# Kernel tuning notes

Measured on AMD Instinct MI355X. Metric: run time of the kernel, lower is better.

## Reference

```python
import jax, jax.numpy as jnp
import numpy as np

NUM_HEADS = 4

def setup_inputs() -> dict:
    key = jax.random.key(0)
    ks = jax.random.split(key, 5)
    B, T, F, C = 2, 128, 256, 256
    # weights scaled ~1/sqrt(C) so softmax is not saturated
    s = 1.0 / np.sqrt(C)
    return {
        "x": jax.random.normal(ks[0], (B, T, F, C), jnp.float32),
        "w_in": jax.random.normal(ks[1], (3 * C, C), jnp.float32) * s,
        "b_in": jax.random.normal(ks[2], (3 * C,), jnp.float32) * 0.01,
        "w_out": jax.random.normal(ks[3], (C, C), jnp.float32) * s,
        "b_out": jax.random.normal(ks[4], (C,), jnp.float32) * 0.01,
        "band": 16,
    }

def reference(x, w_in, b_in, w_out, b_out, band):
    B, T, F, C = x.shape
    H = NUM_HEADS
    D = C // H
    x2 = x.reshape(B * T, F, C)  # attention over frequency, independent per (B,T)
    qkv = x2 @ w_in.T + b_in  # [BT, F, 3C]
    q, k, v = jnp.split(qkv, 3, axis=-1)
    def heads(t):
        return t.reshape(B * T, F, H, D).transpose(0, 2, 1, 3)  # [BT, H, F, D]
    q, k, v = heads(q), heads(k), heads(v)
    scores = jnp.einsum('bhid,bhjd->bhij', q, k) / jnp.sqrt(jnp.asarray(D, x.dtype))
    i = jnp.arange(F)[:, None]
    j = jnp.arange(F)[None, :]
    keep = jnp.abs(i - j) <= band  # banded locality mask [F, F]
    scores = jnp.where(keep, scores, -jnp.inf)
    attn = jax.nn.softmax(scores, axis=-1)
    out = jnp.einsum('bhij,bhjd->bhid', attn, v)  # [BT, H, F, D]
    out = out.transpose(0, 2, 1, 3).reshape(B * T, F, C)
    y = out @ w_out.T + b_out
    return y.reshape(B, T, F, C)
```

## Files before the change

kernel.cpp:

```cpp
#include <hip/hip_runtime.h>
#include <hip/hip_bf16.h>
#include <cstdint>

typedef unsigned int u32;
typedef __attribute__((ext_vector_type(8))) __bf16 bf16x8;
typedef __attribute__((ext_vector_type(4))) float f32x4;
typedef __attribute__((ext_vector_type(2))) _Float16 half2_t;

#define BT_N 256
#define F_N 256
#define C_N 256
#define H_N 4
#define D_N 64
#define TC_N 768
#define M_N (BT_N * F_N)

__device__ __forceinline__ ushort f2bf(float f) {
  u32 u = __float_as_uint(f);
  u32 r = (u + 0x7fffu + ((u >> 16) & 1u)) >> 16;
  return (ushort)r;
}

__device__ __forceinline__ half2_t u2h(u32 u) {
  return __builtin_bit_cast(half2_t, u);
}

__device__ __forceinline__ void store_out(_Float16* p, float v) { *p = (_Float16)v; }
__device__ __forceinline__ void store_out(float* p, float v) { *p = v; }

__device__ __forceinline__ void gload_lds16(const ushort* g, ushort* l) {
  __builtin_amdgcn_global_load_lds(
      (const __attribute__((address_space(1))) u32*)g,
      (__attribute__((address_space(3))) u32*)l, 16, 0, 0);
}

__device__ __forceinline__ float dpp_xor1_add(float x) {
  int t = __builtin_amdgcn_mov_dpp(__builtin_bit_cast(int, x), 0xB1, 0xF, 0xF, true);
  return x + __builtin_bit_cast(float, t);
}
__device__ __forceinline__ float dpp_xor2_add(float x) {
  int t = __builtin_amdgcn_mov_dpp(__builtin_bit_cast(int, x), 0x4E, 0xF, 0xF, true);
  return x + __builtin_bit_cast(float, t);
}

__global__ __launch_bounds__(256) void cvt3_f32_bf16_k(
    const float* __restrict__ sx, ushort* __restrict__ dx, int nx4,
    const float* __restrict__ si, ushort* __restrict__ di, int ni4,
    const float* __restrict__ so, ushort* __restrict__ dq, int no4) {
  int idx = blockIdx.x * 256 + threadIdx.x;
  int stride = gridDim.x * 256;
  int ntot = nx4 + ni4 + no4;
  for (int i = idx; i < ntot; i += stride) {
    const float4* s;
    ushort* d;
    if (i < nx4) { s = (const float4*)sx + i; d = dx + (size_t)i * 4; }
    else if (i < nx4 + ni4) { int k = i - nx4; s = (const float4*)si + k; d = di + (size_t)k * 4; }
    else { int k = i - nx4 - ni4; s = (const float4*)so + k; d = dq + (size_t)k * 4; }
    float4 v = *s;
    u32 a = (u32)f2bf(v.x) | ((u32)f2bf(v.y) << 16);
    u32 b = (u32)f2bf(v.z) | ((u32)f2bf(v.w) << 16);
    *(uint2*)d = make_uint2(a, b);
  }
}

template <typename OutT>
__global__ __launch_bounds__(256, 2) void gemm_bt(
    const ushort* __restrict__ Ap, const ushort* __restrict__ Bp,
    const float* __restrict__ bias, OutT* __restrict__ Cp,
    int N, int NTN, int nwg8) {
  constexpr bool F32OUT = (sizeof(OutT) == 4);
  constexpr int SMEM_BYTES = F32OUT ? 67584 : 65536;
  __shared__ char smem[SMEM_BYTES];
  ushort* smemH = (ushort*)smem;

  const int tid = threadIdx.x;
  const int lane = tid & 63;
  const int wid = tid >> 6;
  const int wr = wid >> 1, wc = wid & 1;
  const int l15 = lane & 15, l4 = lane >> 4;
  const int b = blockIdx.x;
  const int bid = (b & 7) * nwg8 + (b >> 3);
  const int tm = bid / NTN;
  const int tn = bid - tm * NTN;
  const int rowBase = tm * 128, colBase = tn * 128;

  f32x4 acc[4][4] = {};

  const int ar = (tid >> 3);
  const int akk = (((tid & 7) ^ (ar & 7)) << 3);
  const ushort* gA = Ap + (size_t)(rowBase + ar) * 256 + akk;
  const ushort* gB = Bp + (size_t)(colBase + ar) * 256 + akk;

#define STAGE(buf, k0)                                                        \
  {                                                                           \
    ushort* As_ = smemH + (buf) * 8192;                                       \
    ushort* Bs_ = smemH + 16384 + (buf) * 8192;                               \
    _Pragma("unroll") for (int c = 0; c < 4; ++c) {                           \
      gload_lds16(gA + (size_t)(c * 32) * 256 + (k0),                         \
                  As_ + (size_t)(c * 256 + (wid << 6)) * 8);                  \
      gload_lds16(gB + (size_t)(c * 32) * 256 + (k0),                         \
                  Bs_ + (size_t)(c * 256 + (wid << 6)) * 8);                  \
    }                                                                         \
  }

  STAGE(0, 0);
  int cur = 0;
#pragma unroll
  for (int t = 0; t < 4; ++t) {
    __syncthreads();
    if (t < 3) STAGE(cur ^ 1, (t + 1) * 64);
    const ushort* As_ = smemH + cur * 8192;
    const ushort* Bs_ = smemH + 16384 + cur * 8192;
#pragma unroll
    for (int kk = 0; kk < 2; ++kk) {
      bf16x8 af[4];
      bf16x8 bfr[4];
#pragma unroll
      for (int i2 = 0; i2 < 4; ++i2) {
        int row = wr * 64 + i2 * 16 + l15;
        af[i2] = *(const bf16x8*)(As_ + row * 64 + (((kk * 4 + l4) ^ (l15 & 7)) * 8));
      }
#pragma unroll
      for (int j2 = 0; j2 < 4; ++j2) {
        int row = wc * 64 + j2 * 16 + l15;
        bfr[j2] = *(const bf16x8*)(Bs_ + row * 64 + (((kk * 4 + l4) ^ (l15 & 7)) * 8));
      }
#pragma unroll
      for (int i2 = 0; i2 < 4; ++i2)
#pragma unroll
        for (int j2 = 0; j2 < 4; ++j2)
          acc[i2][j2] = __builtin_amdgcn_mfma_f32_16x16x32_bf16(
              af[i2], bfr[j2], acc[i2][j2], 0, 0, 0);
    }
    cur ^= 1;
  }
#undef STAGE

  __syncthreads();
  if constexpr (F32OUT) {
    float* eb = (float*)smem;
#pragma unroll
    for (int j2 = 0; j2 < 4; ++j2) {
      float bv = bias[colBase + wc * 64 + j2 * 16 + l15];
#pragma unroll
      for (int i2 = 0; i2 < 4; ++i2)
#pragma unroll
        for (int r = 0; r < 4; ++r)
          eb[(wr * 64 + i2 * 16 + l4 * 4 + r) * 132 + wc * 64 + j2 * 16 + l15] =
              acc[i2][j2][r] + bv;
    }
    __syncthreads();
#pragma unroll
    for (int i = 0; i < 32; ++i) {
      int row = wid * 32 + i;
      uint2 d = *(const uint2*)((const u32*)eb + row * 132 + lane * 2);
      *(uint2*)((float*)Cp + (size_t)(rowBase + row) * N + colBase + lane * 2) = d;
    }
  } else {
    ushort* eb = smemH;
#pragma unroll
    for (int j2 = 0; j2 < 4; ++j2) {
      float bv = bias[colBase + wc * 64 + j2 * 16 + l15];
#pragma unroll
      for (int i2 = 0; i2 < 4; ++i2)
#pragma unroll
        for (int r = 0; r < 4; ++r) {
          _Float16 h = (_Float16)(acc[i2][j2][r] + bv);
          eb[(wr * 64 + i2 * 16 + l4 * 4 + r) * 136 + wc * 64 + j2 * 16 + l15] =
              __builtin_bit_cast(ushort, h);
        }
    }
    __syncthreads();
#pragma unroll
    for (int i = 0; i < 16; ++i) {
      int row = wid * 32 + 2 * i + (lane >> 5);
      int hl = lane & 31;
      uint2 d = *(const uint2*)(eb + row * 136 + hl * 4);
      *(uint2*)((_Float16*)Cp + (size_t)(rowBase + row) * N + colBase + hl * 4) = d;
    }
  }
}

__global__ __launch_bounds__(256) void attn_banded(
    const _Float16* __restrict__ qkv, ushort* __restrict__ aout) {
  __shared__ uint4 kbuf4[256 * 8];
  __shared__ uint4 vbuf4[256 * 8];
  const int tid = threadIdx.x;
  const int bt = blockIdx.x >> 2;
  const int h = blockIdx.x & 3;
  const _Float16* base = qkv + (size_t)bt * F_N * TC_N + h * D_N;

  {
    const int r0 = tid >> 3;
    const int c = tid & 7;
    const int cs = c ^ ((tid >> 5) & 7);
#pragma unroll
    for (int p = 0; p < 8; ++p) {
      int r = p * 32 + r0;
      uint4 k4 = *(const uint4*)(base + (size_t)r * TC_N + 256 + c * 8);
      uint4 v4 = *(const uint4*)(base + (size_t)r * TC_N + 512 + c * 8);
      kbuf4[r * 8 + cs] = k4;
      vbuf4[r * 8 + cs] = v4;
    }
  }

  const int q = tid >> 2;
  const int s = tid & 3;

  half2_t qh[4][8];
#pragma unroll
  for (int ii = 0; ii < 4; ++ii) {
    const uint4* gq = (const uint4*)(base + (size_t)(4 * q + ii) * TC_N + s * 16);
    uint4 a = gq[0], b2 = gq[1];
    qh[ii][0] = u2h(a.x); qh[ii][1] = u2h(a.y); qh[ii][2] = u2h(a.z); qh[ii][3] = u2h(a.w);
    qh[ii][4] = u2h(b2.x); qh[ii][5] = u2h(b2.y); qh[ii][6] = u2h(b2.z); qh[ii][7] = u2h(b2.w);
  }
  __syncthreads();

  float l[4] = {0.f, 0.f, 0.f, 0.f};
  half2_t o[4][8];
  const _Float16 z0 = (_Float16)0.f;
#pragma unroll
  for (int ii = 0; ii < 4; ++ii)
#pragma unroll
    for (int m = 0; m < 8; ++m) o[ii][m] = half2_t{z0, z0};

#pragma unroll 4
  for (int jo = 0; jo < 36; ++jo) {
    int j = 4 * q - 16 + jo;
    int jc = j < 0 ? 0 : (j > 255 ? 255 : j);
    int cb = (jc >> 2) & 7;
    const uint4* krow = kbuf4 + jc * 8;
    uint4 ka = krow[(2 * s) ^ cb];
    uint4 kb = krow[(2 * s + 1) ^ cb];
    half2_t kh[8];
    kh[0] = u2h(ka.x); kh[1] = u2h(ka.y); kh[2] = u2h(ka.z); kh[3] = u2h(ka.w);
    kh[4] = u2h(kb.x); kh[5] = u2h(kb.y); kh[6] = u2h(kb.z); kh[7] = u2h(kb.w);

    float dv[4];
#pragma unroll
    for (int ii = 0; ii < 4; ++ii) {
      float a0 = 0.f, a1 = 0.f;
#pragma unroll
      for (int m = 0; m < 4; ++m) {
        a0 = __builtin_amdgcn_fdot2(kh[2 * m], qh[ii][2 * m], a0, false);
        a1 = __builtin_amdgcn_fdot2(kh[2 * m + 1], qh[ii][2 * m + 1], a1, false);
      }
      dv[ii] = a0 + a1;
    }
#pragma unroll
    for (int ii = 0; ii < 4; ++ii) {
      dv[ii] = dpp_xor1_add(dv[ii]);
      dv[ii] = dpp_xor2_add(dv[ii]);
    }

    bool okj = (j >= 0) && (j < 256);
    float p[4];
    p[0] = (okj && jo <= 32) ? __expf(dv[0] * 0.125f) : 0.f;
    p[1] = (okj && jo >= 1 && jo <= 33) ? __expf(dv[1] * 0.125f) : 0.f;
    p[2] = (okj && jo >= 2 && jo <= 34) ? __expf(dv[2] * 0.125f) : 0.f;
    p[3] = (okj && jo >= 3) ? __expf(dv[3] * 0.125f) : 0.f;

    const uint4* vrow = vbuf4 + jc * 8;
    uint4 va = vrow[(2 * s) ^ cb];
    uint4 vb = vrow[(2 * s + 1) ^ cb];
    half2_t vh[8];
    vh[0] = u2h(va.x); vh[1] = u2h(va.y); vh[2] = u2h(va.z); vh[3] = u2h(va.w);
    vh[4] = u2h(vb.x); vh[5] = u2h(vb.y); vh[6] = u2h(vb.z); vh[7] = u2h(vb.w);

#pragma unroll
    for (int ii = 0; ii < 4; ++ii) {
      l[ii] += p[ii];
      _Float16 pf = (_Float16)p[ii];
      half2_t ph = {pf, pf};
#pragma unroll
      for (int m = 0; m < 8; ++m) o[ii][m] = vh[m] * ph + o[ii][m];
    }
  }

#pragma unroll
  for (int ii = 0; ii < 4; ++ii) {
    float inv = 1.f / l[ii];
    u32 w[4];
#pragma unroll
    for (int m = 0; m < 4; ++m) {
      float f0 = (float)o[ii][2 * m][0] * inv;
      float f1 = (float)o[ii][2 * m][1] * inv;
      float f2 = (float)o[ii][2 * m + 1][0] * inv;
      float f3 = (float)o[ii][2 * m + 1][1] * inv;
      w[m] = 0;
      w[m] = (u32)f2bf(f0) | ((u32)f2bf(f1) << 16);
      ((u32*)w)[m] = w[m];
      u32 hi = (u32)f2bf(f2) | ((u32)f2bf(f3) << 16);
      if (m & 1) { }
      w[m] = w[m];
      u32* dst = (u32*)(aout + (size_t)(bt * F_N + 4 * q + ii) * C_N + h * D_N + s * 16) + 2 * m;
      dst[0] = w[m];
      dst[1] = hi;
    }
  }
}

extern "C" void kernel_launch(void* const* d_in, const int* in_sizes, int n_in,
                              void* d_out, int out_size, void* d_ws, size_t ws_size,
                              hipStream_t stream) {
  const float* x = (const float*)d_in[0];
  const float* w_in = (const float*)d_in[1];
  const float* b_in = (const float*)d_in[2];
  const float* w_out = (const float*)d_in[3];
  const float* b_out = (const float*)d_in[4];
  float* y = (float*)d_out;

  char* ws = (char*)d_ws;
  const size_t qkv_bytes = (size_t)M_N * TC_N * 2;
  const size_t xb_bytes = (size_t)M_N * C_N * 2;
  _Float16* qkv = (_Float16*)ws;
  ushort* xb = (ushort*)(ws + qkv_bytes);
  ushort* attn = xb;
  ushort* winb = (ushort*)(ws + qkv_bytes + xb_bytes);
  ushort* woutb = winb + TC_N * C_N;

  cvt3_f32_bf16_k<<<2048, 256, 0, stream>>>(x, xb, M_N * C_N / 4,
                                            w_in, winb, TC_N * C_N / 4,
                                            w_out, woutb, C_N * C_N / 4);

  gemm_bt<_Float16><<<(M_N / 128) * (TC_N / 128), 256, 0, stream>>>(
      xb, winb, b_in, qkv, TC_N, TC_N / 128, (M_N / 128) * (TC_N / 128) / 8);

  attn_banded<<<BT_N * H_N, 256, 0, stream>>>(qkv, attn);

  gemm_bt<float><<<(M_N / 128) * (C_N / 128), 256, 0, stream>>>(
      attn, woutb, b_out, y, C_N, C_N / 128, (M_N / 128) * (C_N / 128) / 8);
}
```

Measured before the change: 120.5 us.

## Rewrite banded attention kernel with MFMA 16x16x16 f16 tiles

Replaces the scalar fdot2 banded attention with a matrix-core version. Each wave handles 64 query rows as four 16-row tiles, computes QK^T over three 16-key tiles covering the band with MFMA, and applies a precomputed bitmask, exp2 with folded scale, and a shuffle-reduced row sum. V is stored transposed in LDS so P·V can also use MFMA. This computes some wasted products outside the band and adds transposed scalar LDS stores, but it moves the main arithmetic onto matrix cores.

```diff
diff --git a/kernel.cpp b/kernel.cpp
--- a/kernel.cpp
+++ b/kernel.cpp
@@ -6,6 +6,8 @@
 typedef __attribute__((ext_vector_type(8))) __bf16 bf16x8;
 typedef __attribute__((ext_vector_type(4))) float f32x4;
 typedef __attribute__((ext_vector_type(2))) _Float16 half2_t;
+typedef __attribute__((ext_vector_type(4))) _Float16 half4;
+typedef __attribute__((ext_vector_type(2))) __fp16 fp16x2;
 
 #define BT_N 256
 #define F_N 256
@@ -14,6 +16,7 @@
 #define D_N 64
 #define TC_N 768
 #define M_N (BT_N * F_N)
+#define VT_ST 268
 
 __device__ __forceinline__ ushort f2bf(float f) {
   u32 u = __float_as_uint(f);
@@ -21,26 +24,10 @@
   return (ushort)r;
 }
 
-__device__ __forceinline__ half2_t u2h(u32 u) {
-  return __builtin_bit_cast(half2_t, u);
-}
-
-__device__ __forceinline__ void store_out(_Float16* p, float v) { *p = (_Float16)v; }
-__device__ __forceinline__ void store_out(float* p, float v) { *p = v; }
-
 __device__ __forceinline__ void gload_lds16(const ushort* g, ushort* l) {
   __builtin_amdgcn_global_load_lds(
       (const __attribute__((address_space(1))) u32*)g,
       (__attribute__((address_space(3))) u32*)l, 16, 0, 0);
-}
-
-__device__ __forceinline__ float dpp_xor1_add(float x) {
-  int t = __builtin_amdgcn_mov_dpp(__builtin_bit_cast(int, x), 0xB1, 0xF, 0xF, true);
-  return x + __builtin_bit_cast(float, t);
-}
-__device__ __forceinline__ float dpp_xor2_add(float x) {
-  int t = __builtin_amdgcn_mov_dpp(__builtin_bit_cast(int, x), 0x4E, 0xF, 0xF, true);
-  return x + __builtin_bit_cast(float, t);
 }
 
 __global__ __launch_bounds__(256) void cvt3_f32_bf16_k(
@@ -181,122 +168,126 @@
   }
 }
 
-__global__ __launch_bounds__(256) void attn_banded(
+__global__ __launch_bounds__(256) void attn_mfma(
     const _Float16* __restrict__ qkv, ushort* __restrict__ aout) {
-  __shared__ uint4 kbuf4[256 * 8];
-  __shared__ uint4 vbuf4[256 * 8];
+  __shared__ ushort smem[18432 + 64 * VT_ST];
   const int tid = threadIdx.x;
   const int bt = blockIdx.x >> 2;
   const int h = blockIdx.x & 3;
-  const _Float16* base = qkv + (size_t)bt * F_N * TC_N + h * D_N;
+  const _Float16* base = qkv + (size_t)bt * 256 * 768 + h * 64;
+  ushort* klds = smem;
+  ushort* vlds = smem + 18432;
 
   {
-    const int r0 = tid >> 3;
-    const int c = tid & 7;
-    const int cs = c ^ ((tid >> 5) & 7);
+    const int r0 = tid >> 3, c8 = tid & 7;
 #pragma unroll
     for (int p = 0; p < 8; ++p) {
-      int r = p * 32 + r0;
-      uint4 k4 = *(const uint4*)(base + (size_t)r * TC_N + 256 + c * 8);
-      uint4 v4 = *(const uint4*)(base + (size_t)r * TC_N + 512 + c * 8);
-      kbuf4[r * 8 + cs] = k4;
-      vbuf4[r * 8 + cs] = v4;
-    }
-  }
-
-  const int q = tid >> 2;
-  const int s = tid & 3;
-
-  half2_t qh[4][8];
-#pragma unroll
-  for (int ii = 0; ii < 4; ++ii) {
-    const uint4* gq = (const uint4*)(base + (size_t)(4 * q + ii) * TC_N + s * 16);
-    uint4 a = gq[0], b2 = gq[1];
-    qh[ii][0] = u2h(a.x); qh[ii][1] = u2h(a.y); qh[ii][2] = u2h(a.z); qh[ii][3] = u2h(a.w);
-    qh[ii][4] = u2h(b2.x); qh[ii][5] = u2h(b2.y); qh[ii][6] = u2h(b2.z); qh[ii][7] = u2h(b2.w);
-  }
+      int j = p * 32 + r0;
+      const uint4 k4 = *(const uint4*)(base + (size_t)j * 768 + 256 + c8 * 8);
+      *(uint4*)(klds + j * 72 + c8 * 8) = k4;
+      const uint4 v4 = *(const uint4*)(base + (size_t)j * 768 + 512 + c8 * 8);
+      const ushort* vh = (const ushort*)&v4;
+      ushort* vtp = vlds + (c8 * 8) * VT_ST + j;
+#pragma unroll
+      for (int i = 0; i < 8; ++i) vtp[i * VT_ST] = vh[i];
+    }
+  }
+
+  const int w = tid >> 6, lane = tid & 63;
+  const int l15 = lane & 15, g = lane >> 4, g4 = g * 4;
+
+  uint2 qf0[4], qf1[4], qf2[4], qf3[4];
+  {
+    const uint2* q0 = (const uint2*)(base + (size_t)(w * 64 + 0 * 16 + l15) * 768 + g4);
+    const uint2* q1 = (const uint2*)(base + (size_t)(w * 64 + 1 * 16 + l15) * 768 + g4);
+    const uint2* q2 = (const uint2*)(base + (size_t)(w * 64 + 2 * 16 + l15) * 768 + g4);
+    const uint2* q3 = (const uint2*)(base + (size_t)(w * 64 + 3 * 16 + l15) * 768 + g4);
+#pragma unroll
+    for (int ks = 0; ks < 4; ++ks) {
+      qf0[ks] = q0[ks * 4]; qf1[ks] = q1[ks * 4];
+      qf2[ks] = q2[ks * 4]; qf3[ks] = q3[ks * 4];
+    }
+  }
+
+  u32 bb = 0;
+#pragma unroll
+  for (int jt = 0; jt < 3; ++jt)
+#pragma unroll
+    for (int r = 0; r < 4; ++r) {
+      int d = 16 * jt + g4 + r - 16 - l15;
+      if (d >= -16 && d <= 16) bb |= 1u << (jt * 4 + r);
+    }
+
   __syncthreads();
 
-  float l[4] = {0.f, 0.f, 0.f, 0.f};
-  half2_t o[4][8];
-  const _Float16 z0 = (_Float16)0.f;
-#pragma unroll
-  for (int ii = 0; ii < 4; ++ii)
-#pragma unroll
-    for (int m = 0; m < 8; ++m) o[ii][m] = half2_t{z0, z0};
-
-#pragma unroll 4
-  for (int jo = 0; jo < 36; ++jo) {
-    int j = 4 * q - 16 + jo;
-    int jc = j < 0 ? 0 : (j > 255 ? 255 : j);
-    int cb = (jc >> 2) & 7;
-    const uint4* krow = kbuf4 + jc * 8;
-    uint4 ka = krow[(2 * s) ^ cb];
-    uint4 kb = krow[(2 * s + 1) ^ cb];
-    half2_t kh[8];
-    kh[0] = u2h(ka.x); kh[1] = u2h(ka.y); kh[2] = u2h(ka.z); kh[3] = u2h(ka.w);
-    kh[4] = u2h(kb.x); kh[5] = u2h(kb.y); kh[6] = u2h(kb.z); kh[7] = u2h(kb.w);
-
-    float dv[4];
-#pragma unroll
-    for (int ii = 0; ii < 4; ++ii) {
-      float a0 = 0.f, a1 = 0.f;
-#pragma unroll
-      for (int m = 0; m < 4; ++m) {
-        a0 = __builtin_amdgcn_fdot2(kh[2 * m], qh[ii][2 * m], a0, false);
-        a1 = __builtin_amdgcn_fdot2(kh[2 * m + 1], qh[ii][2 * m + 1], a1, false);
-      }
-      dv[ii] = a0 + a1;
-    }
-#pragma unroll
-    for (int ii = 0; ii < 4; ++ii) {
-      dv[ii] = dpp_xor1_add(dv[ii]);
-      dv[ii] = dpp_xor2_add(dv[ii]);
-    }
-
-    bool okj = (j >= 0) && (j < 256);
-    float p[4];
-    p[0] = (okj && jo <= 32) ? __expf(dv[0] * 0.125f) : 0.f;
-    p[1] = (okj && jo >= 1 && jo <= 33) ? __expf(dv[1] * 0.125f) : 0.f;
-    p[2] = (okj && jo >= 2 && jo <= 34) ? __expf(dv[2] * 0.125f) : 0.f;
-    p[3] = (okj && jo >= 3) ? __expf(dv[3] * 0.125f) : 0.f;
-
-    const uint4* vrow = vbuf4 + jc * 8;
-    uint4 va = vrow[(2 * s) ^ cb];
-    uint4 vb = vrow[(2 * s + 1) ^ cb];
-    half2_t vh[8];
-    vh[0] = u2h(va.x); vh[1] = u2h(va.y); vh[2] = u2h(va.z); vh[3] = u2h(va.w);
-    vh[4] = u2h(vb.x); vh[5] = u2h(vb.y); vh[6] = u2h(vb.z); vh[7] = u2h(vb.w);
-
-#pragma unroll
-    for (int ii = 0; ii < 4; ++ii) {
-      l[ii] += p[ii];
-      _Float16 pf = (_Float16)p[ii];
-      half2_t ph = {pf, pf};
-#pragma unroll
-      for (int m = 0; m < 8; ++m) o[ii][m] = vh[m] * ph + o[ii][m];
-    }
-  }
-
-#pragma unroll
-  for (int ii = 0; ii < 4; ++ii) {
-    float inv = 1.f / l[ii];
-    u32 w[4];
-#pragma unroll
-    for (int m = 0; m < 4; ++m) {
-      float f0 = (float)o[ii][2 * m][0] * inv;
-      float f1 = (float)o[ii][2 * m][1] * inv;
-      float f2 = (float)o[ii][2 * m + 1][0] * inv;
-      float f3 = (float)o[ii][2 * m + 1][1] * inv;
-      w[m] = 0;
-      w[m] = (u32)f2bf(f0) | ((u32)f2bf(f1) << 16);
-      ((u32*)w)[m] = w[m];
-      u32 hi = (u32)f2bf(f2) | ((u32)f2bf(f3) << 16);
-      if (m & 1) { }
-      w[m] = w[m];
-      u32* dst = (u32*)(aout + (size_t)(bt * F_N + 4 * q + ii) * C_N + h * D_N + s * 16) + 2 * m;
-      dst[0] = w[m];
-      dst[1] = hi;
+  const float SC = 0.18033688f;
+
+#pragma unroll
+  for (int rt = 0; rt < 4; ++rt) {
+    const int R0 = w * 64 + rt * 16;
+    const int Jc = R0 - 16;
+    const uint2* qf = (rt == 0) ? qf0 : (rt == 1) ? qf1 : (rt == 2) ? qf2 : qf3;
+
+    f32x4 st[3] = {};
+#pragma unroll
+    for (int jt = 0; jt < 3; ++jt) {
+      int krow = Jc + 16 * jt + l15;
+      krow = krow < 0 ? 0 : (krow > 255 ? 255 : krow);
+      const ushort* kp = klds + krow * 72 + g4;
+#pragma unroll
+      for (int ks = 0; ks < 4; ++ks) {
+        uint2 kf = *(const uint2*)(kp + ks * 16);
+        st[jt] = __builtin_amdgcn_mfma_f32_16x16x16f16(
+            __builtin_bit_cast(half4, kf), __builtin_bit_cast(half4, qf[ks]),
+            st[jt], 0, 0, 0);
+      }
+    }
+
+    float l_acc = 0.f;
+    float pp[3][4];
+#pragma unroll
+    for (int jt = 0; jt < 3; ++jt)
+#pragma unroll
+      for (int r = 0; r < 4; ++r) {
+        int jg = Jc + 16 * jt + g4 + r;
+        bool keep = (((bb >> (jt * 4 + r)) & 1u) != 0) && (jg >= 0) && (jg < 256);
+        float pv = keep ? __builtin_amdgcn_exp2f(st[jt][r] * SC) : 0.f;
+        pp[jt][r] = pv;
+        l_acc += pv;
+      }
+    l_acc += __shfl_xor(l_acc, 16, 64);
+    l_acc += __shfl_xor(l_acc, 32, 64);
+    const float inv = 1.f / l_acc;
+
+    uint2 pf[3];
+#pragma unroll
+    for (int jt = 0; jt < 3; ++jt) {
+      fp16x2 a = __builtin_amdgcn_cvt_pkrtz(pp[jt][0] * inv, pp[jt][1] * inv);
+      fp16x2 c = __builtin_amdgcn_cvt_pkrtz(pp[jt][2] * inv, pp[jt][3] * inv);
+      pf[jt].x = __builtin_bit_cast(u32, a);
+      pf[jt].y = __builtin_bit_cast(u32, c);
+    }
+
+    f32x4 ot[4] = {};
+#pragma unroll
+    for (int kt = 0; kt < 3; ++kt) {
+      int jb = Jc + 16 * kt + g4;
+      jb = jb < 0 ? 0 : (jb > 252 ? 252 : jb);
+#pragma unroll
+      for (int mt = 0; mt < 4; ++mt) {
+        uint2 vfr = *(const uint2*)(vlds + (16 * mt + l15) * VT_ST + jb);
+        ot[mt] = __builtin_amdgcn_mfma_f32_16x16x16f16(
+            __builtin_bit_cast(half4, vfr), __builtin_bit_cast(half4, pf[kt]),
+            ot[mt], 0, 0, 0);
+      }
+    }
+
+    ushort* orow = aout + (size_t)(bt * 256 + R0 + l15) * 256 + h * 64 + g4;
+#pragma unroll
+    for (int mt = 0; mt < 4; ++mt) {
+      u32 lo = (u32)f2bf(ot[mt][0]) | ((u32)f2bf(ot[mt][1]) << 16);
+      u32 hi = (u32)f2bf(ot[mt][2]) | ((u32)f2bf(ot[mt][3]) << 16);
+      *(uint2*)(orow + mt * 16) = make_uint2(lo, hi);
     }
   }
 }
@@ -327,7 +318,7 @@
   gemm_bt<_Float16><<<(M_N / 128) * (TC_N / 128), 256, 0, stream>>>(
       xb, winb, b_in, qkv, TC_N, TC_N / 128, (M_N / 128) * (TC_N / 128) / 8);
 
-  attn_banded<<<BT_N * H_N, 256, 0, stream>>>(qkv, attn);
+  attn_mfma<<<BT_N * H_N, 256, 0, stream>>>(qkv, attn);
 
   gemm_bt<float><<<(M_N / 128) * (C_N / 128), 256, 0, stream>>>(
       attn, woutb, b_out, y, C_N, C_N / 128, (M_N / 128) * (C_N / 128) / 8);
```

New measurement: 102.9 us. -14.6%, faster.
